# Kernel tuning notes

Measured on AMD Instinct MI355X. Metric: run time of the kernel, lower is better.

The kernel has to match this reference:

```python
import jax, jax.numpy as jnp
import numpy as np

B, L, U, H = 32, 2048, 512, 8
HD = U // H  # head_dim = 64


def _conv1d(x, w, b, pad):
    # x: (B, Cin, L), w: (Cout, Cin, K) -> (B, Cout, L)
    y = jax.lax.conv_general_dilated(
        x, w, window_strides=(1,), padding=[(pad, pad)],
        dimension_numbers=("NCH", "OIH", "NCH"))
    return y + b[None, :, None]


def _maxpool1d_k3(x):
    # kernel=3, stride=1, pad=1, same as nn.MaxPool1d(3,1,1)
    return jax.lax.reduce_window(
        x, -jnp.inf, jax.lax.max,
        window_dimensions=(1, 1, 3), window_strides=(1, 1, 1),
        padding=[(0, 0), (0, 0), (1, 1)])


def setup_inputs() -> dict:
    key = jax.random.key(0)
    ks = jax.random.split(key, 12)
    s = 0.02
    return {
        "t": jax.random.normal(ks[0], (B, L, U), jnp.float32),
        "g": jax.random.normal(ks[1], (B, 1, U), jnp.float32),
        "g_mask": jnp.ones((B, 1), jnp.int32),
        "t_mask": jax.random.randint(ks[2], (B, L), 0, 2).astype(jnp.int32),
        "Wq": jax.random.normal(ks[3], (U, U, 3), jnp.float32) * s,
        "bq": jnp.zeros((U,), jnp.float32),
        "Wk": jax.random.normal(ks[4], (U, U, 3), jnp.float32) * s,
        "bk": jnp.zeros((U,), jnp.float32),
        "Wv": jax.random.normal(ks[5], (U, U, 3), jnp.float32) * s,
        "bv": jnp.zeros((U,), jnp.float32),
        "Wh": jax.random.normal(ks[6], (H, H, 1), jnp.float32) * s,
        "bh": jnp.zeros((H,), jnp.float32),
        "Wo": jax.random.normal(ks[7], (U, U, 1), jnp.float32) * s,
        "bo": jnp.zeros((U,), jnp.float32),
    }


def reference(t, g, g_mask, t_mask, Wq, bq, Wk, bk, Wv, bv, Wh, bh, Wo, bo):
    x = t.transpose(0, 2, 1)                      # (B, U, L)
    q = _conv1d(x, Wq, bq, 1)                     # (B, U, L)
    k = _conv1d(x, Wk, bk, 1)
    v = _conv1d(x, Wv, bv, 1)

    # global query: max over sequence -> (B, H, 1, HD)
    q_ = q.max(-1).reshape(B, H, 1, HD)
    # keys: [global max key, maxpooled local keys] -> (B, H, 1+L, HD)
    k_g = k.max(-1).reshape(B, H, 1, HD)
    k_c = _maxpool1d_k3(k).reshape(B, H, HD, L).transpose(0, 1, 3, 2)
    key_ = jnp.concatenate([k_g, k_c], axis=2)
    v_g = v.max(-1).reshape(B, H, 1, HD)
    v_c = _maxpool1d_k3(v).reshape(B, H, HD, L).transpose(0, 1, 3, 2)
    value_ = jnp.concatenate([v_g, v_c], axis=2)

    attn = jnp.einsum("bhqd,bhkd->bhqk", q_, key_) / jnp.sqrt(jnp.float32(U))
    key_mask = jnp.concatenate([g_mask, t_mask], axis=-1)  # (B, 1+L)
    attn = jnp.where(key_mask[:, None, None, :] == 0, -jnp.inf, attn)
    attn = jax.nn.softmax(attn, axis=-1)
    # query mask multiply (g_mask broadcast over heads & keys)
    attn = attn * g_mask[:, None, :, None].astype(jnp.float32)

    out = jnp.einsum("bhqk,bhkd->bhqd", attn, value_)  # (B, H, 1, HD)
    out = out.reshape(B, H, HD)
    # conv1d_h: 1x1 conv mixing heads
    out = jnp.einsum("oi,bid->bod", Wh[:, :, 0], out) + bh[None, :, None]
    out = out.reshape(B, H, 1, HD).transpose(0, 2, 1, 3).reshape(B, 1, U)
    # conv1d_out: 1x1 conv over channels
    out = jnp.einsum("oi,bqi->bqo", Wo[:, :, 0], out) + bo
    return out  # (B, 1, U)
```

## Files before the change

### kernel.cpp

```cpp
#include <hip/hip_runtime.h>
#include <hip/hip_fp16.h>

#define B_  32
#define L_  2048
#define U_  512
#define H_  8
#define HD_ 64

typedef __attribute__((ext_vector_type(8))) _Float16 half8;
typedef __attribute__((ext_vector_type(4))) float f32x4;

__device__ __forceinline__ unsigned fmap(float x) {
    unsigned u = __float_as_uint(x);
    return (u & 0x80000000u) ? ~u : (u | 0x80000000u);
}
__device__ __forceinline__ float funmap(unsigned m) {
    unsigned bits = (m & 0x80000000u) ? (m ^ 0x80000000u) : ~m;
    return __uint_as_float(bits);
}

__global__ void __launch_bounds__(256) t_cvt(const float* __restrict__ t,
                                             __half* __restrict__ t16) {
    const size_t id = (size_t)blockIdx.x * 256 + threadIdx.x;
    const float4 a = *(const float4*)(t + id * 8);
    const float4 b = *(const float4*)(t + id * 8 + 4);
    auto p0 = __builtin_amdgcn_cvt_pkrtz(a.x, a.y);
    auto p1 = __builtin_amdgcn_cvt_pkrtz(a.z, a.w);
    auto p2 = __builtin_amdgcn_cvt_pkrtz(b.x, b.y);
    auto p3 = __builtin_amdgcn_cvt_pkrtz(b.z, b.w);
    half8 hv;
    hv[0] = p0[0]; hv[1] = p0[1]; hv[2] = p1[0]; hv[3] = p1[1];
    hv[4] = p2[0]; hv[5] = p2[1]; hv[6] = p3[0]; hv[7] = p3[1];
    *(half8*)(t16 + id * 8) = hv;
}

__global__ void repack_w2(const float* __restrict__ Wq,
                          const float* __restrict__ Wk,
                          const float* __restrict__ Wv,
                          __half* __restrict__ Wrp2) {
    int id = blockIdx.x * 256 + threadIdx.x;
    int mb2  = id / 12288;
    int rem  = id % 12288;
    int F    = rem >> 6;
    int lane = rem & 63;
    int mblk = mb2 >> 1, wm = mb2 & 1;
    int mi = F & 3, ks = (F >> 2) & 1, t3 = F >> 3;
    int kk = t3 % 3, iblk = t3 / 3;
    int mat = mblk >> 2;
    const float* W = (mat == 0) ? Wq : (mat == 1) ? Wk : Wv;
    int ol = ((mblk & 3) << 7) + wm * 64 + mi * 16 + (lane & 15);
    int ib = iblk * 64 + ks * 32 + (lane >> 4) * 8;
    half8 hv;
#pragma unroll
    for (int j = 0; j < 8; ++j)
        hv[j] = (_Float16)W[(ol * 512 + ib + j) * 3 + kk];
    *(half8*)(Wrp2 + (size_t)id * 8) = hv;
}

__global__ void wot_repack(const float* __restrict__ Wo, float* __restrict__ WoT) {
    int id = blockIdx.x * 256 + threadIdx.x;
    int o = id & 511, i = id >> 9;
    WoT[(size_t)i * 512 + o] = Wo[(size_t)o * 512 + i];
}

__global__ void __launch_bounds__(256, 3) conv_gemm(
    const __half* __restrict__ t16,
    const __half* __restrict__ Wrp2,
    const float* __restrict__ bq,
    const float* __restrict__ bk,
    const float* __restrict__ bv,
    __half* __restrict__ kbuf, __half* __restrict__ vbuf,
    unsigned* __restrict__ qmaxU, unsigned* __restrict__ kmaxU,
    unsigned* __restrict__ vmaxU) {
    __shared__ __align__(16) __half lB16[2][130 * 64];

    const int tid  = threadIdx.x;
    const int lane = tid & 63;
    const int w    = tid >> 6;
    const int wm = w >> 1, wn = w & 1;
    const int xcd  = blockIdx.x & 7;
    const int slot = blockIdx.x >> 3;
    const int g    = slot / 384;
    const int r    = slot % 384;
    const int chunk= r / 6;
    const int mblk = g * 6 + (r % 6);
    const int ntile= xcd + 8 * chunk;
    const int bb = ntile >> 4;
    const int l0 = (ntile & 15) << 7;
    const int lane15 = lane & 15, kgrp = lane >> 4;

    const char* Abase = (const char*)Wrp2 + (size_t)(mblk * 2 + wm) * 196608;
    const __half* tB = t16 + (size_t)bb * L_ * U_;

    f32x4 acc[4][4];
#pragma unroll
    for (int a = 0; a < 4; ++a)
#pragma unroll
        for (int c = 0; c < 4; ++c) acc[a][c] = (f32x4){0.f, 0.f, 0.f, 0.f};

    auto stageB = [&](int nb, int buf) {
        const int i0 = nb << 6;
#pragma unroll
        for (int d = 0; d < 4; ++d) {
            const int rowb = w * 32 + d * 8;
            const int row  = rowb + (lane >> 3);
            const int l    = l0 - 1 + row;
            const int p8   = lane & 7;
            const char* g2 = (const char*)(tB + (size_t)l * U_ + i0) + ((p8 ^ (l & 7)) << 4);
            if (l >= 0 && l < L_)
                __builtin_amdgcn_global_load_lds(
                    (const __attribute__((address_space(1))) unsigned int*)g2,
                    (__attribute__((address_space(3))) unsigned int*)((char*)lB16[buf] + rowb * 128),
                    16, 0, 0);
        }
        if (w == 0 && lane < 16) {
            const int row = 128 + (lane >> 3);
            const int l   = l0 - 1 + row;
            const int p8  = lane & 7;
            const char* g2 = (const char*)(tB + (size_t)l * U_ + i0) + ((p8 ^ (l & 7)) << 4);
            if (l >= 0 && l < L_)
                __builtin_amdgcn_global_load_lds(
                    (const __attribute__((address_space(1))) unsigned int*)g2,
                    (__attribute__((address_space(3))) unsigned int*)((char*)lB16[buf] + 128 * 128),
                    16, 0, 0);
        }
    };

    if (l0 == 0 && tid < 64) {
        lB16[0][tid] = (__half)0.f; lB16[1][tid] = (__half)0.f;
    }
    if (l0 == 1920 && tid < 64) {
        lB16[0][129 * 64 + tid] = (__half)0.f; lB16[1][129 * 64 + tid] = (__half)0.f;
    }

    stageB(0, 0);
    __syncthreads();

    for (int iblk = 0; iblk < 8; ++iblk) {
        const int cur = iblk & 1;
        const char* bbase = (const char*)lB16[cur];
#pragma unroll
        for (int kk = 0; kk < 3; ++kk) {
#pragma unroll
            for (int ks = 0; ks < 2; ++ks) {
                half8 af[4];
#pragma unroll
                for (int mi = 0; mi < 4; ++mi)
                    af[mi] = *(const half8*)(Abase +
                        ((((size_t)iblk * 3 + kk) * 2 + ks) * 4 + mi) * 1024 + lane * 16);
                if (kk == 0 && ks == 0 && iblk < 7) stageB(iblk + 1, cur ^ 1);
                half8 bfr[4];
#pragma unroll
                for (int ni = 0; ni < 4; ++ni) {
                    const int rbuf = wn * 64 + ni * 16 + lane15 + kk;
                    const int key  = (rbuf + 7) & 7;
                    const int p    = ks * 4 + kgrp;
                    bfr[ni] = *(const half8*)(bbase + rbuf * 128 + ((p ^ key) << 4));
                }
#pragma unroll
                for (int mi = 0; mi < 4; ++mi)
#pragma unroll
                    for (int ni = 0; ni < 4; ++ni)
                        acc[mi][ni] = __builtin_amdgcn_mfma_f32_16x16x32_f16(
                            af[mi], bfr[ni], acc[mi][ni], 0, 0, 0);
            }
        }
        __syncthreads();
    }

    const int mat = mblk >> 2;
    const float* bias = (mat == 0) ? bq : (mat == 1) ? bk : bv;
    const int oBase = ((mblk & 3) << 7) + wm * 64 + kgrp * 4;
#pragma unroll
    for (int mi = 0; mi < 4; ++mi) {
#pragma unroll
        for (int r2 = 0; r2 < 4; ++r2) {
            const int o = oBase + mi * 16 + r2;
            const float bsv = bias[o];
            float vals[4];
            float mx = -3.0e38f;
#pragma unroll
            for (int ni = 0; ni < 4; ++ni) {
                float v = acc[mi][ni][r2] + bsv;
                vals[ni] = v;
                mx = fmaxf(mx, v);
            }
#pragma unroll
            for (int d = 1; d < 16; d <<= 1) mx = fmaxf(mx, __shfl_xor(mx, d, 64));
            if (mat == 0) {
                if (lane15 == 0) atomicMax(&qmaxU[bb * U_ + o], fmap(mx));
            } else {
                __half* buf = (mat == 1) ? kbuf : vbuf;
                size_t rowbase = ((size_t)bb * U_ + o) * L_ + l0 + wn * 64;
#pragma unroll
                for (int ni = 0; ni < 4; ++ni)
                    buf[rowbase + ni * 16 + lane15] = __float2half(vals[ni]);
                unsigned* mptr = (mat == 1) ? kmaxU : vmaxU;
                if (lane15 == 0) atomicMax(&mptr[bb * U_ + o], fmap(mx));
            }
        }
    }
}

__global__ void __launch_bounds__(1024) attn_kernel(
    const __half* __restrict__ kbuf, const __half* __restrict__ vbuf,
    const unsigned* __restrict__ qmaxU, const unsigned* __restrict__ kmaxU,
    const unsigned* __restrict__ vmaxU,
    const int* __restrict__ g_mask, const int* __restrict__ t_mask,
    float* __restrict__ attout) {
    const int bh = blockIdx.x;
    const int b = bh >> 3, h = bh & 7;
    const int tid = threadIdx.x;
    const int lane = tid & 63;
    const int wid = tid >> 6;
    __shared__ float qs[64], kg[64], vg[64];
    __shared__ float pl[2048];
    __shared__ float wredA[16], wredB[16];
    if (tid < 64) {
        qs[tid] = funmap(qmaxU[b * U_ + h * 64 + tid]);
        kg[tid] = funmap(kmaxU[b * U_ + h * 64 + tid]);
        vg[tid] = funmap(vmaxU[b * U_ + h * 64 + tid]);
    }
    __syncthreads();
    const float scale = 0.044194173824159216f;

    const __half* kbase = kbuf + ((size_t)b * U_ + h * 64) * L_;
    const int l0 = tid * 2;
    const int offm = (l0 == 0) ? 0 : l0 - 2;
    const int offp = (l0 + 2 >= L_) ? L_ - 2 : l0 + 2;
    const bool mE = (l0 == 0), pE = (l0 + 2 >= L_);
    float acc0 = 0.f, acc1 = 0.f;
    {
        const __half* pr = kbase;
#pragma unroll 4
        for (int o = 0; o < 64; ++o) {
            const __half2 hm = *(const __half2*)(pr + offm);
            const __half2 hc = *(const __half2*)(pr + l0);
            const __half2 hp = *(const __half2*)(pr + offp);
            const float fL = mE ? -3.0e38f : __half2float(hm.y);
            const float f1 = __half2float(hc.x), f2 = __half2float(hc.y);
            const float fR = pE ? -3.0e38f : __half2float(hp.x);
            const float qw = qs[o];
            acc0 += qw * fmaxf(fL, fmaxf(f1, f2));
            acc1 += qw * fmaxf(f1, fmaxf(f2, fR));
            pr += L_;
        }
    }
    float lg0, lg1;
    {
        const int tm0 = t_mask[b * L_ + l0], tm1 = t_mask[b * L_ + l0 + 1];
        lg0 = (tm0 == 0) ? -INFINITY : acc0 * scale;
        lg1 = (tm1 == 0) ? -INFINITY : acc1 * scale;
    }
    float lmax = fmaxf(lg0, lg1);
#pragma unroll
    for (int d = 1; d < 64; d <<= 1) lmax = fmaxf(lmax, __shfl_xor(lmax, d, 64));
    if (lane == 0) wredA[wid] = lmax;
    float ag = 0.f;
#pragma unroll 8
    for (int d = 0; d < 64; ++d) ag += qs[d] * kg[d];
    const int gm = g_mask[b];
    const float lgg = gm ? ag * scale : -INFINITY;
    __syncthreads();
    float mx = lgg;
#pragma unroll
    for (int i = 0; i < 16; ++i) mx = fmaxf(mx, wredA[i]);
    const float e0 = (lg0 <= -3.0e38f) ? 0.f : __expf(lg0 - mx);
    const float e1 = (lg1 <= -3.0e38f) ? 0.f : __expf(lg1 - mx);
    pl[l0] = e0; pl[l0 + 1] = e1;
    float psum = e0 + e1;
#pragma unroll
    for (int d = 1; d < 64; d <<= 1) psum += __shfl_xor(psum, d, 64);
    if (lane == 0) wredB[wid] = psum;
    __syncthreads();
    const float eg = gm ? __expf(lgg - mx) : 0.f;
    float den = eg;
#pragma unroll
    for (int i = 0; i < 16; ++i) den += wredB[i];
    if (!(den > 0.f)) den = 1.f;
    const int o = tid >> 4;
    const int ch = tid & 15;
    const __half* vrow = vbuf + ((size_t)b * U_ + h * 64 + o) * L_;
    float s = 0.f;
#pragma unroll 2
    for (int it = 0; it < 16; ++it) {
        const int lb = it * 128 + ch * 8;
        union { uint4 u; __half hh[8]; } pk;
        pk.u = *(const uint4*)(vrow + lb);
        float f[10];
#pragma unroll
        for (int j = 0; j < 8; ++j) f[j + 1] = __half2float(pk.hh[j]);
        f[0] = (lb == 0) ? -3.0e38f : __half2float(vrow[lb - 1]);
        f[9] = (lb + 8 >= L_) ? -3.0e38f : __half2float(vrow[lb + 8]);
#pragma unroll
        for (int j = 0; j < 8; ++j)
            s += pl[lb + j] * fmaxf(f[j], fmaxf(f[j + 1], f[j + 2]));
    }
#pragma unroll
    for (int d = 1; d < 16; d <<= 1) s += __shfl_xor(s, d, 64);
    if (ch == 0) {
        float val = (eg * vg[o] + s) / den;
        val *= (float)gm;
        attout[(size_t)b * U_ + h * 64 + o] = val;
    }
}

__global__ void __launch_bounds__(512) out_kernel(
    const float* __restrict__ attout,
    const float* __restrict__ Wh, const float* __restrict__ bh,
    const float* __restrict__ WoT, const float* __restrict__ bo,
    float* __restrict__ out) {
    const int b = blockIdx.x;
    const int tid = threadIdx.x;
    __shared__ float tmp[512];
    const int oh = tid >> 6, d = tid & 63;
    float s = bh[oh];
#pragma unroll
    for (int i = 0; i < 8; ++i)
        s += Wh[oh * 8 + i] * attout[b * U_ + i * 64 + d];
    tmp[oh * 64 + d] = s;
    __syncthreads();
    float s2 = bo[tid];
    for (int i = 0; i < 512; ++i) s2 += WoT[i * 512 + tid] * tmp[i];
    out[b * U_ + tid] = s2;
}

extern "C" void kernel_launch(void* const* d_in, const int* in_sizes, int n_in,
                              void* d_out, int out_size, void* d_ws, size_t ws_size,
                              hipStream_t stream) {
    const float* t  = (const float*)d_in[0];
    const int* g_mask = (const int*)d_in[2];
    const int* t_mask = (const int*)d_in[3];
    const float* Wq = (const float*)d_in[4];
    const float* bq = (const float*)d_in[5];
    const float* Wk = (const float*)d_in[6];
    const float* bk = (const float*)d_in[7];
    const float* Wv = (const float*)d_in[8];
    const float* bv = (const float*)d_in[9];
    const float* Wh = (const float*)d_in[10];
    const float* bh = (const float*)d_in[11];
    const float* Wo = (const float*)d_in[12];
    const float* bo = (const float*)d_in[13];

    char* ws = (char*)d_ws;
    __half* Wrp2 = (__half*)ws;
    float* WoT   = (float*)(ws + 4718592);
    __half* t16  = (__half*)(ws + 5767168);
    __half* kbuf = (__half*)(ws + 5767168 + 67108864);
    __half* vbuf = (__half*)(ws + 5767168 + 2 * 67108864);
    unsigned* qmaxU = (unsigned*)(ws + 5767168 + 3 * 67108864);
    unsigned* kmaxU = qmaxU + 16384;
    unsigned* vmaxU = kmaxU + 16384;
    float* attout = (float*)(vmaxU + 16384);

    (void)hipMemsetAsync(qmaxU, 0, 3 * 16384 * sizeof(unsigned), stream);
    t_cvt<<<16384, 256, 0, stream>>>(t, t16);
    repack_w2<<<1152, 256, 0, stream>>>(Wq, Wk, Wv, Wrp2);
    wot_repack<<<1024, 256, 0, stream>>>(Wo, WoT);
    conv_gemm<<<6144, 256, 0, stream>>>(t16, Wrp2, bq, bk, bv, kbuf, vbuf,
                                        qmaxU, kmaxU, vmaxU);
    attn_kernel<<<256, 1024, 0, stream>>>(kbuf, vbuf, qmaxU, kmaxU, vmaxU,
                                          g_mask, t_mask, attout);
    out_kernel<<<32, 512, 0, stream>>>(attout, Wh, bh, WoT, bo, (float*)d_out);
}
```

Before: 594.0 us.

## Merge prep kernels with memset, widen attn key loads, split output GEMV

Merges the weight repack, the Wo transpose and the zeroing of the max buffers into one prep kernel, removing a memset and two launches. The attention logit loop now reads the left and centre key pairs with a single 8-byte load instead of two 4-byte loads. The output kernel is split across 8 blocks per batch, each computing 64 outputs with an 8-way partial reduction in shared memory, so the final GEMV gets more parallelism. These are small overhead reductions next to the dominant conv GEMM.

```diff
diff --git a/kernel.cpp b/kernel.cpp
--- a/kernel.cpp
+++ b/kernel.cpp
@@ -9,6 +9,8 @@
 
 typedef __attribute__((ext_vector_type(8))) _Float16 half8;
 typedef __attribute__((ext_vector_type(4))) float f32x4;
+
+struct __align__(4) H4 { __half2 lo, hi; };
 
 __device__ __forceinline__ unsigned fmap(float x) {
     unsigned u = __float_as_uint(x);
@@ -34,33 +36,38 @@
     *(half8*)(t16 + id * 8) = hv;
 }
 
-__global__ void repack_w2(const float* __restrict__ Wq,
-                          const float* __restrict__ Wk,
-                          const float* __restrict__ Wv,
-                          __half* __restrict__ Wrp2) {
-    int id = blockIdx.x * 256 + threadIdx.x;
-    int mb2  = id / 12288;
-    int rem  = id % 12288;
-    int F    = rem >> 6;
-    int lane = rem & 63;
-    int mblk = mb2 >> 1, wm = mb2 & 1;
-    int mi = F & 3, ks = (F >> 2) & 1, t3 = F >> 3;
-    int kk = t3 % 3, iblk = t3 / 3;
-    int mat = mblk >> 2;
-    const float* W = (mat == 0) ? Wq : (mat == 1) ? Wk : Wv;
-    int ol = ((mblk & 3) << 7) + wm * 64 + mi * 16 + (lane & 15);
-    int ib = iblk * 64 + ks * 32 + (lane >> 4) * 8;
-    half8 hv;
-#pragma unroll
-    for (int j = 0; j < 8; ++j)
-        hv[j] = (_Float16)W[(ol * 512 + ib + j) * 3 + kk];
-    *(half8*)(Wrp2 + (size_t)id * 8) = hv;
-}
-
-__global__ void wot_repack(const float* __restrict__ Wo, float* __restrict__ WoT) {
-    int id = blockIdx.x * 256 + threadIdx.x;
-    int o = id & 511, i = id >> 9;
-    WoT[(size_t)i * 512 + o] = Wo[(size_t)o * 512 + i];
+__global__ void __launch_bounds__(256) prep(
+    const float* __restrict__ Wq, const float* __restrict__ Wk,
+    const float* __restrict__ Wv, __half* __restrict__ Wrp2,
+    const float* __restrict__ Wo, float* __restrict__ WoT,
+    unsigned* __restrict__ maxU ) {
+    const int blk = blockIdx.x;
+    if (blk < 1152) {
+        int id = blk * 256 + threadIdx.x;
+        int mb2  = id / 12288;
+        int rem  = id % 12288;
+        int F    = rem >> 6;
+        int lane = rem & 63;
+        int mblk = mb2 >> 1, wm = mb2 & 1;
+        int mi = F & 3, ks = (F >> 2) & 1, t3 = F >> 3;
+        int kk = t3 % 3, iblk = t3 / 3;
+        int mat = mblk >> 2;
+        const float* W = (mat == 0) ? Wq : (mat == 1) ? Wk : Wv;
+        int ol = ((mblk & 3) << 7) + wm * 64 + mi * 16 + (lane & 15);
+        int ib = iblk * 64 + ks * 32 + (lane >> 4) * 8;
+        half8 hv;
+#pragma unroll
+        for (int j = 0; j < 8; ++j)
+            hv[j] = (_Float16)W[(ol * 512 + ib + j) * 3 + kk];
+        *(half8*)(Wrp2 + (size_t)id * 8) = hv;
+    } else if (blk < 2176) {
+        int id = (blk - 1152) * 256 + threadIdx.x;
+        int o = id & 511, i = id >> 9;
+        WoT[(size_t)i * 512 + o] = Wo[(size_t)o * 512 + i];
+    } else {
+        int id = (blk - 2176) * 256 + threadIdx.x;
+        maxU[id] = 0u; maxU[id + 16384] = 0u; maxU[id + 32768] = 0u;
+    }
 }
 
 __global__ void __launch_bounds__(256, 3) conv_gemm(
@@ -226,19 +233,19 @@
 
     const __half* kbase = kbuf + ((size_t)b * U_ + h * 64) * L_;
     const int l0 = tid * 2;
-    const int offm = (l0 == 0) ? 0 : l0 - 2;
-    const int offp = (l0 + 2 >= L_) ? L_ - 2 : l0 + 2;
     const bool mE = (l0 == 0), pE = (l0 + 2 >= L_);
+    const int offm2 = mE ? 0 : l0 - 2;
+    const int offp  = pE ? L_ - 2 : l0 + 2;
     float acc0 = 0.f, acc1 = 0.f;
     {
         const __half* pr = kbase;
 #pragma unroll 4
         for (int o = 0; o < 64; ++o) {
-            const __half2 hm = *(const __half2*)(pr + offm);
-            const __half2 hc = *(const __half2*)(pr + l0);
+            const H4 w4 = *(const H4*)(pr + offm2);
             const __half2 hp = *(const __half2*)(pr + offp);
-            const float fL = mE ? -3.0e38f : __half2float(hm.y);
-            const float f1 = __half2float(hc.x), f2 = __half2float(hc.y);
+            const float f1 = mE ? __half2float(w4.lo.x) : __half2float(w4.hi.x);
+            const float f2 = mE ? __half2float(w4.lo.y) : __half2float(w4.hi.y);
+            const float fL = mE ? -3.0e38f : __half2float(w4.lo.y);
             const float fR = pE ? -3.0e38f : __half2float(hp.x);
             const float qw = qs[o];
             acc0 += qw * fmaxf(fL, fmaxf(f1, f2));
@@ -310,19 +317,35 @@
     const float* __restrict__ Wh, const float* __restrict__ bh,
     const float* __restrict__ WoT, const float* __restrict__ bo,
     float* __restrict__ out) {
-    const int b = blockIdx.x;
+    const int b  = blockIdx.x >> 3;
+    const int chk = blockIdx.x & 7;
     const int tid = threadIdx.x;
     __shared__ float tmp[512];
-    const int oh = tid >> 6, d = tid & 63;
-    float s = bh[oh];
-#pragma unroll
-    for (int i = 0; i < 8; ++i)
-        s += Wh[oh * 8 + i] * attout[b * U_ + i * 64 + d];
-    tmp[oh * 64 + d] = s;
-    __syncthreads();
-    float s2 = bo[tid];
-    for (int i = 0; i < 512; ++i) s2 += WoT[i * 512 + tid] * tmp[i];
-    out[b * U_ + tid] = s2;
+    __shared__ float part[8][64];
+    {
+        const int oh = tid >> 6, d = tid & 63;
+        float s = bh[oh];
+#pragma unroll
+        for (int i = 0; i < 8; ++i)
+            s += Wh[oh * 8 + i] * attout[b * U_ + i * 64 + d];
+        tmp[oh * 64 + d] = s;
+    }
+    __syncthreads();
+    const int p  = tid >> 6;
+    const int ol = tid & 63;
+    const int o  = chk * 64 + ol;
+    float s2 = 0.f;
+#pragma unroll 8
+    for (int i = p * 64; i < p * 64 + 64; ++i)
+        s2 += WoT[(size_t)i * 512 + o] * tmp[i];
+    part[p][ol] = s2;
+    __syncthreads();
+    if (tid < 64) {
+        float tot = bo[chk * 64 + tid];
+#pragma unroll
+        for (int q = 0; q < 8; ++q) tot += part[q][tid];
+        out[b * U_ + chk * 64 + tid] = tot;
+    }
 }
 
 extern "C" void kernel_launch(void* const* d_in, const int* in_sizes, int n_in,
@@ -353,13 +376,11 @@
     unsigned* vmaxU = kmaxU + 16384;
     float* attout = (float*)(vmaxU + 16384);
 
-    (void)hipMemsetAsync(qmaxU, 0, 3 * 16384 * sizeof(unsigned), stream);
+    prep<<<2240, 256, 0, stream>>>(Wq, Wk, Wv, Wrp2, Wo, WoT, qmaxU);
     t_cvt<<<16384, 256, 0, stream>>>(t, t16);
-    repack_w2<<<1152, 256, 0, stream>>>(Wq, Wk, Wv, Wrp2);
-    wot_repack<<<1024, 256, 0, stream>>>(Wo, WoT);
     conv_gemm<<<6144, 256, 0, stream>>>(t16, Wrp2, bq, bk, bv, kbuf, vbuf,
                                         qmaxU, kmaxU, vmaxU);
     attn_kernel<<<256, 1024, 0, stream>>>(kbuf, vbuf, qmaxU, kmaxU, vmaxU,
                                           g_mask, t_mask, attout);
-    out_kernel<<<32, 512, 0, stream>>>(attout, Wh, bh, WoT, bo, (float*)d_out);
-}
+    out_kernel<<<256, 512, 0, stream>>>(attout, Wh, bh, WoT, bo, (float*)d_out);
+}
```

Measured after the change: 595.7 us. About the same (+0.3%).
